# Kernel optimization log

Hardware: AMD Instinct MI355X
Metric: run time of the kernel (lower is better)

## Reference

```python
import jax, jax.numpy as jnp
import numpy as np

B, TH, TS, HS, WS = 16, 1024, 1024, 1024, 1024


def setup_inputs() -> dict:
    key = jax.random.key(0)
    k1, k2, k3, k4 = jax.random.split(key, 4)
    h = jax.random.normal(k1, (B, TH, HS), dtype=jnp.float32)
    s = jax.random.normal(k2, (B, TS, WS), dtype=jnp.float32)
    # nn.Linear params: weight [out, in], bias [out]
    Wh = jax.random.normal(k3, (HS, HS), dtype=jnp.float32) * 0.02
    bh = jnp.zeros((HS,), dtype=jnp.float32)
    Ws = jax.random.normal(k4, (HS, WS), dtype=jnp.float32) * 0.02
    bs = jnp.zeros((HS,), dtype=jnp.float32)
    return {"h": h, "s": s, "Wh": Wh, "bh": bh, "Ws": Ws, "bs": bs}


def reference(h, s, Wh, bh, Ws, bs):
    hp = jnp.einsum('bth,oh->bto', h, Wh) + bh          # [B, TH, HS]
    sp = jnp.einsum('btw,ow->bto', s, Ws) + bs          # [B, TS, HS]
    scores = jnp.einsum('bik,bjk->bij', hp, sp)         # [B, TH, TS]
    b, th, _ = scores.shape
    # faithful to torch: flat-chunk into rows of length TH, softmax over dim 1
    sm = jax.nn.softmax(scores.reshape(-1, th), axis=1).reshape(b, -1, th)  # [B, TS, TH]
    res = jnp.matmul(sm, hp)                            # [B, TS, HS]
    return res.reshape(-1, res.shape[-1])               # [B*TS, HS]
```

## Files before the change

### kernel.cpp

```cpp
#include <hip/hip_runtime.h>
#include <hip/hip_bf16.h>
#include <stdint.h>


typedef _Float16 half_t;
typedef __attribute__((ext_vector_type(8))) _Float16 half8;
typedef __attribute__((ext_vector_type(4))) _Float16 half4;
typedef __attribute__((ext_vector_type(4))) float floatx4;

__device__ __forceinline__ void gl2lds16(const void* g, void* l) {
    __builtin_amdgcn_global_load_lds(
        (const __attribute__((address_space(1))) uint32_t*)(uintptr_t)g,
        (__attribute__((address_space(3))) uint32_t*)(uintptr_t)l,
        16, 0, 0);
}

#define NT16 16

template<int WF32, int WH16, int WH16T>
__global__ __launch_bounds__(512, 2) void gemm256(
    const half_t* __restrict__ A, const half_t* __restrict__ B,
    const float* __restrict__ bias,
    float* __restrict__ Cf, half_t* __restrict__ Ch, half_t* __restrict__ ChT,
    int lda, int ldb, int N,
    long aBatch, long bBatch, long cfBatch, int ldcf)
{
    extern __shared__ char smem[];

    const int tid  = threadIdx.x;
    const int wave = tid >> 6;
    const int lane = tid & 63;
    const int wr = wave >> 2;
    const int wc = wave & 3;
    const int lr = lane & 15, lg = lane >> 4;

    const long batch = blockIdx.z;
    const half_t* Ab = A + batch * aBatch;
    const half_t* Bb = B + batch * bBatch;
    const int row0 = blockIdx.x * 256;
    const int col0 = blockIdx.y * 256;

    floatx4 acc[8][4];
#pragma unroll
    for (int m = 0; m < 8; ++m)
#pragma unroll
        for (int n = 0; n < 4; ++n)
            acc[m][n] = (floatx4){0.f, 0.f, 0.f, 0.f};

    long aOff[2][2], bOff[2][2];
#pragma unroll
    for (int hh = 0; hh < 2; ++hh)
#pragma unroll
        for (int i = 0; i < 2; ++i) {
            const int off = hh * 16384 + i * 8192 + tid * 16;
            const int e = off ^ (((off >> 7) & 7) << 4);
            const int r = e >> 7, cb = e & 127;
            aOff[hh][i] = (long)(row0 + r) * (long)(lda * 2) + cb;
            bOff[hh][i] = (long)(col0 + r) * (long)(ldb * 2) + cb;
        }

    const int wave_s = __builtin_amdgcn_readfirstlane(wave);
    auto stageHalf = [&](int buf, int isA, int hh, int kk) {
#pragma unroll
        for (int i = 0; i < 2; ++i) {
            const char* g = (isA ? (const char*)Ab + aOff[hh][i]
                                 : (const char*)Bb + bOff[hh][i]) + (long)kk * 2;
            gl2lds16(g, smem + buf * 65536 + (isA ? 0 : 32768)
                          + hh * 16384 + i * 8192 + wave_s * 1024);
        }
    };

    uint32_t aof0 = (uint32_t)((wr * 128 + lr) * 128 + ((lg * 16) ^ ((lr & 7) << 4)));
    uint32_t aof1 = (uint32_t)((wr * 128 + lr) * 128 + ((64 + lg * 16) ^ ((lr & 7) << 4)));
    uint32_t bof0 = (uint32_t)(32768 + (wc * 64 + lr) * 128 + ((lg * 16) ^ ((lr & 7) << 4)));
    uint32_t bof1 = (uint32_t)(32768 + (wc * 64 + lr) * 128 + ((64 + lg * 16) ^ ((lr & 7) << 4)));

    stageHalf(0, 1, 0, 0);  stageHalf(0, 1, 1, 0);
    stageHalf(0, 0, 0, 0);  stageHalf(0, 0, 1, 0);
    __syncthreads();

    for (int t = 0; t < NT16; ++t) {
        if (t + 1 < NT16) {
            const int nxt = (t & 1) ^ 1;
            const int k1 = (t + 1) * 64;
            stageHalf(nxt, 1, 0, k1);  stageHalf(nxt, 1, 1, k1);
            stageHalf(nxt, 0, 0, k1);  stageHalf(nxt, 0, 1, k1);
        }

        half8 aF[4][2], bF[4][2];
#pragma unroll
        for (int ni = 0; ni < 4; ++ni) {
            bF[ni][0] = *(const half8*)(smem + bof0 + ni * 2048);
            bF[ni][1] = *(const half8*)(smem + bof1 + ni * 2048);
        }
#pragma unroll
        for (int mi = 0; mi < 4; ++mi) {
            aF[mi][0] = *(const half8*)(smem + aof0 + mi * 2048);
            aF[mi][1] = *(const half8*)(smem + aof1 + mi * 2048);
        }
#pragma unroll
        for (int mi = 0; mi < 4; ++mi)
#pragma unroll
            for (int ni = 0; ni < 4; ++ni)
#pragma unroll
                for (int ks = 0; ks < 2; ++ks)
                    acc[mi][ni] = __builtin_amdgcn_mfma_f32_16x16x32_f16(
                        aF[mi][ks], bF[ni][ks], acc[mi][ni], 0, 0, 0);
#pragma unroll
        for (int mi = 0; mi < 4; ++mi) {
            aF[mi][0] = *(const half8*)(smem + aof0 + (4 + mi) * 2048);
            aF[mi][1] = *(const half8*)(smem + aof1 + (4 + mi) * 2048);
        }
#pragma unroll
        for (int mi = 0; mi < 4; ++mi)
#pragma unroll
            for (int ni = 0; ni < 4; ++ni)
#pragma unroll
                for (int ks = 0; ks < 2; ++ks)
                    acc[4 + mi][ni] = __builtin_amdgcn_mfma_f32_16x16x32_f16(
                        aF[mi][ks], bF[ni][ks], acc[4 + mi][ni], 0, 0, 0);

        __syncthreads();
        aof0 ^= 65536; aof1 ^= 65536; bof0 ^= 65536; bof1 ^= 65536;
    }

    {
        float* wlds = (float*)(smem + wave * 2304);
        float bv[4];
#pragma unroll
        for (int n = 0; n < 4; ++n)
            bv[n] = bias ? bias[col0 + wc * 64 + n * 16 + lr] : 0.f;
        const int er = lane >> 2, ec = lane & 3;
        const int oc = lane >> 1, tc = lane & 1;
#pragma unroll
        for (int m = 0; m < 8; ++m) {
#pragma unroll
            for (int np = 0; np < 2; ++np) {
#pragma unroll
                for (int n2 = 0; n2 < 2; ++n2)
#pragma unroll
                    for (int j = 0; j < 4; ++j)
                        wlds[(lg * 4 + j) * 36 + n2 * 16 + lr] =
                            acc[m][np * 2 + n2][j] + bv[np * 2 + n2];
                const int grow = row0 + wr * 128 + m * 16;
                const int gcol = col0 + wc * 64 + np * 32;
                float4 q0 = *(float4*)&wlds[er * 36 + ec * 8];
                float4 q1 = *(float4*)&wlds[er * 36 + ec * 8 + 4];
                if (WF32) {
                    float* p = Cf + batch * cfBatch + (long)(grow + er) * ldcf + gcol + ec * 8;
                    *(float4*)p = q0;
                    *(float4*)(p + 4) = q1;
                }
                if (WH16) {
                    half8 o = { (half_t)q0.x, (half_t)q0.y, (half_t)q0.z, (half_t)q0.w,
                                (half_t)q1.x, (half_t)q1.y, (half_t)q1.z, (half_t)q1.w };
                    *(half8*)&Ch[(long)(grow + er) * N + gcol + ec * 8] = o;
                }
                if (WH16T) {
                    float tv[8];
#pragma unroll
                    for (int k = 0; k < 8; ++k)
                        tv[k] = wlds[(tc * 8 + k) * 36 + oc];
                    half8 o = { (half_t)tv[0], (half_t)tv[1], (half_t)tv[2], (half_t)tv[3],
                                (half_t)tv[4], (half_t)tv[5], (half_t)tv[6], (half_t)tv[7] };
                    const int gt = grow + tc * 8;
                    *(half8*)&ChT[(long)(gt >> 10) * 1048576
                                  + (long)(gcol + oc) * 1024 + (gt & 1023)] = o;
                }
                __builtin_amdgcn_s_waitcnt(0);
            }
        }
    }
}

__global__ void softmax_inplace(float* __restrict__ S) {
    const long r = blockIdx.x;
    float* row = S + r * 1024;
    const int tid = threadIdx.x;
    const int wave = tid >> 6, lane = tid & 63;

    float4 v = ((const float4*)row)[tid];
    float mx = fmaxf(fmaxf(v.x, v.y), fmaxf(v.z, v.w));
#pragma unroll
    for (int off = 32; off > 0; off >>= 1)
        mx = fmaxf(mx, __shfl_xor(mx, off));
    __shared__ float rmx[4], rsm[4];
    if (lane == 0) rmx[wave] = mx;
    __syncthreads();
    mx = fmaxf(fmaxf(rmx[0], rmx[1]), fmaxf(rmx[2], rmx[3]));

    float e0 = __expf(v.x - mx), e1 = __expf(v.y - mx);
    float e2 = __expf(v.z - mx), e3 = __expf(v.w - mx);
    float s = e0 + e1 + e2 + e3;
#pragma unroll
    for (int off = 32; off > 0; off >>= 1)
        s += __shfl_xor(s, off);
    if (lane == 0) rsm[wave] = s;
    __syncthreads();
    s = rsm[0] + rsm[1] + rsm[2] + rsm[3];

    const float inv = 1.0f / s;
    half4 o = { (half_t)(e0 * inv), (half_t)(e1 * inv), (half_t)(e2 * inv), (half_t)(e3 * inv) };
    ((half4*)((half_t*)S + r * 2048))[tid] = o;
}

__global__ void cvt_f16(const float4* __restrict__ src, half4* __restrict__ dst, int n4) {
    const int stride = gridDim.x * blockDim.x;
    for (int i = blockIdx.x * blockDim.x + threadIdx.x; i < n4; i += stride) {
        float4 v = src[i];
        half4 o = { (half_t)v.x, (half_t)v.y, (half_t)v.z, (half_t)v.w };
        dst[i] = o;
    }
}

extern "C" void kernel_launch(void* const* d_in, const int* in_sizes, int n_in,
                              void* d_out, int out_size, void* d_ws, size_t ws_size,
                              hipStream_t stream) {
    const float* h  = (const float*)d_in[0];
    const float* s  = (const float*)d_in[1];
    const float* Wh = (const float*)d_in[2];
    const float* bh = (const float*)d_in[3];
    const float* Ws = (const float*)d_in[4];
    const float* bs = (const float*)d_in[5];

    const long MB = 16384;
    const long D  = 1024;

    char* w = (char*)d_ws;
    half_t* h16 = (half_t*)w;  w += MB * D * 2;
    half_t* s16 = (half_t*)w;  w += MB * D * 2;
    float*  sc  = (float*)h16;
    half_t* Wh16 = (half_t*)w;  w += D * D * 2;
    half_t* Ws16 = (half_t*)w;  w += D * D * 2;
    half_t* hp16 = (half_t*)w;  w += MB * D * 2;
    half_t* sp16 = (half_t*)w;  w += MB * D * 2;
    half_t* hpT  = (half_t*)w;  w += MB * D * 2;

    hipFuncSetAttribute(reinterpret_cast<const void*>(&gemm256<0,1,1>),
                        hipFuncAttributeMaxDynamicSharedMemorySize, 131072);
    hipFuncSetAttribute(reinterpret_cast<const void*>(&gemm256<0,1,0>),
                        hipFuncAttributeMaxDynamicSharedMemorySize, 131072);
    hipFuncSetAttribute(reinterpret_cast<const void*>(&gemm256<1,0,0>),
                        hipFuncAttributeMaxDynamicSharedMemorySize, 131072);

    cvt_f16<<<512,  256, 0, stream>>>((const float4*)Wh, (half4*)Wh16, (int)(D * D / 4));
    cvt_f16<<<512,  256, 0, stream>>>((const float4*)Ws, (half4*)Ws16, (int)(D * D / 4));
    cvt_f16<<<2048, 256, 0, stream>>>((const float4*)h,  (half4*)h16,  (int)(MB * D / 4));
    cvt_f16<<<2048, 256, 0, stream>>>((const float4*)s,  (half4*)s16,  (int)(MB * D / 4));

    gemm256<0,1,1><<<dim3(64, 4, 1), 512, 131072, stream>>>(
        h16, Wh16, bh, nullptr, hp16, hpT, 1024, 1024, 1024, 0, 0, 0, 0);
    gemm256<0,1,0><<<dim3(64, 4, 1), 512, 131072, stream>>>(
        s16, Ws16, bs, nullptr, sp16, nullptr, 1024, 1024, 1024, 0, 0, 0, 0);
    gemm256<1,0,0><<<dim3(4, 4, 16), 512, 131072, stream>>>(
        hp16, sp16, nullptr, sc, nullptr, nullptr, 1024, 1024, 1024,
        1048576L, 1048576L, 1048576L, 1024);
    softmax_inplace<<<16384, 256, 0, stream>>>(sc);
    gemm256<1,0,0><<<dim3(4, 4, 16), 512, 131072, stream>>>(
        (const half_t*)sc, hpT, nullptr, (float*)d_out, nullptr, nullptr,
        2048, 1024, 1024, 2097152L, 1048576L, 1048576L, 1024);
}
```

Before: 236.8 us.

## Fuse fp32-to-fp16 conversion of activations into projection GEMM A-loads and add XCD block swizzle

```diff
diff --git a/kernel.cpp b/kernel.cpp
--- a/kernel.cpp
+++ b/kernel.cpp
@@ -17,9 +17,10 @@
 
 #define NT16 16
 
-template<int WF32, int WH16, int WH16T>
+template<int WF32, int WH16, int WH16T, int RSA, int SWZ>
 __global__ __launch_bounds__(512, 2) void gemm256(
-    const half_t* __restrict__ A, const half_t* __restrict__ B,
+    const half_t* __restrict__ A, const float* __restrict__ A32,
+    const half_t* __restrict__ B,
     const float* __restrict__ bias,
     float* __restrict__ Cf, half_t* __restrict__ Ch, half_t* __restrict__ ChT,
     int lda, int ldb, int N,
@@ -34,11 +35,21 @@
     const int wc = wave & 3;
     const int lr = lane & 15, lg = lane >> 4;
 
-    const long batch = blockIdx.z;
-    const half_t* Ab = A + batch * aBatch;
+    long batch; int row0, col0;
+    if constexpr (SWZ) {
+        const int lin = blockIdx.x + (blockIdx.y << 2) + (blockIdx.z << 4);
+        const int xcd = lin & 7, per = lin >> 3;
+        batch = (xcd << 1) | (per >> 4);
+        const int wt = per & 15;
+        row0 = (wt & 3) * 256;
+        col0 = (wt >> 2) * 256;
+    } else {
+        batch = blockIdx.z;
+        row0 = blockIdx.x * 256;
+        col0 = blockIdx.y * 256;
+    }
+
     const half_t* Bb = B + batch * bBatch;
-    const int row0 = blockIdx.x * 256;
-    const int col0 = blockIdx.y * 256;
 
     floatx4 acc[8][4];
 #pragma unroll
@@ -47,7 +58,8 @@
         for (int n = 0; n < 4; ++n)
             acc[m][n] = (floatx4){0.f, 0.f, 0.f, 0.f};
 
-    long aOff[2][2], bOff[2][2];
+    long bOff[2][2];
+    long aOffG[2][2];
 #pragma unroll
     for (int hh = 0; hh < 2; ++hh)
 #pragma unroll
@@ -55,36 +67,86 @@
             const int off = hh * 16384 + i * 8192 + tid * 16;
             const int e = off ^ (((off >> 7) & 7) << 4);
             const int r = e >> 7, cb = e & 127;
-            aOff[hh][i] = (long)(row0 + r) * (long)(lda * 2) + cb;
             bOff[hh][i] = (long)(col0 + r) * (long)(ldb * 2) + cb;
+            if constexpr (!RSA)
+                aOffG[hh][i] = (long)(row0 + r) * (long)(lda * 2) + cb;
         }
 
     const int wave_s = __builtin_amdgcn_readfirstlane(wave);
-    auto stageHalf = [&](int buf, int isA, int hh, int kk) {
-#pragma unroll
-        for (int i = 0; i < 2; ++i) {
-            const char* g = (isA ? (const char*)Ab + aOff[hh][i]
-                                 : (const char*)Bb + bOff[hh][i]) + (long)kk * 2;
-            gl2lds16(g, smem + buf * 65536 + (isA ? 0 : 32768)
-                          + hh * 16384 + i * 8192 + wave_s * 1024);
-        }
+    auto stageB = [&](int buf, int kk) {
+#pragma unroll
+        for (int hh = 0; hh < 2; ++hh)
+#pragma unroll
+            for (int i = 0; i < 2; ++i)
+                gl2lds16((const char*)Bb + bOff[hh][i] + (long)kk * 2,
+                         smem + buf * 65536 + 32768 + hh * 16384 + i * 8192 + wave_s * 1024);
     };
+    auto stageA16 = [&](int buf, int kk) {
+        const half_t* Ab = A + batch * aBatch;
+#pragma unroll
+        for (int hh = 0; hh < 2; ++hh)
+#pragma unroll
+            for (int i = 0; i < 2; ++i)
+                gl2lds16((const char*)Ab + aOffG[hh][i] + (long)kk * 2,
+                         smem + buf * 65536 + hh * 16384 + i * 8192 + wave_s * 1024);
+    };
+
+    int rsaRow[4], rsaKb[4];
+#pragma unroll
+    for (int c = 0; c < 4; ++c) {
+        const int off = c * 8192 + tid * 16;
+        rsaRow[c] = off >> 7;
+        rsaKb[c]  = off & 127;
+    }
 
     uint32_t aof0 = (uint32_t)((wr * 128 + lr) * 128 + ((lg * 16) ^ ((lr & 7) << 4)));
     uint32_t aof1 = (uint32_t)((wr * 128 + lr) * 128 + ((64 + lg * 16) ^ ((lr & 7) << 4)));
     uint32_t bof0 = (uint32_t)(32768 + (wc * 64 + lr) * 128 + ((lg * 16) ^ ((lr & 7) << 4)));
     uint32_t bof1 = (uint32_t)(32768 + (wc * 64 + lr) * 128 + ((64 + lg * 16) ^ ((lr & 7) << 4)));
 
-    stageHalf(0, 1, 0, 0);  stageHalf(0, 1, 1, 0);
-    stageHalf(0, 0, 0, 0);  stageHalf(0, 0, 1, 0);
+    auto rsaLoad = [&](float4 (&fv)[4][2], int kk) {
+#pragma unroll
+        for (int c = 0; c < 4; ++c) {
+            const float* src = A32 + batch * aBatch
+                             + (long)(row0 + rsaRow[c]) * lda + kk + (rsaKb[c] >> 1);
+            fv[c][0] = *(const float4*)src;
+            fv[c][1] = *(const float4*)(src + 4);
+        }
+    };
+    auto rsaWrite = [&](float4 (&fv)[4][2], int buf) {
+#pragma unroll
+        for (int c = 0; c < 4; ++c) {
+            half8 o = { (half_t)fv[c][0].x, (half_t)fv[c][0].y, (half_t)fv[c][0].z, (half_t)fv[c][0].w,
+                        (half_t)fv[c][1].x, (half_t)fv[c][1].y, (half_t)fv[c][1].z, (half_t)fv[c][1].w };
+            *(half8*)(smem + buf * 65536 + rsaRow[c] * 128
+                      + (rsaKb[c] ^ ((rsaRow[c] & 7) << 4))) = o;
+        }
+    };
+
+    if constexpr (RSA) {
+        float4 fv[4][2];
+        rsaLoad(fv, 0);
+        stageB(0, 0);
+        rsaWrite(fv, 0);
+    } else {
+        stageA16(0, 0);
+        stageB(0, 0);
+    }
     __syncthreads();
 
     for (int t = 0; t < NT16; ++t) {
+        const int nxt = (t & 1) ^ 1;
+        const int k1 = (t + 1) * 64;
+
+        float4 fv[4][2];
         if (t + 1 < NT16) {
-            const int nxt = (t & 1) ^ 1;
-            const int k1 = (t + 1) * 64;
-            stageHalf(nxt, 1, 0, k1);  stageHalf(nxt, 1, 1, k1);
-            stageHalf(nxt, 0, 0, k1);  stageHalf(nxt, 0, 1, k1);
+            if constexpr (RSA) {
+                rsaLoad(fv, k1);
+                stageB(nxt, k1);
+            } else {
+                stageA16(nxt, k1);
+                stageB(nxt, k1);
+            }
         }
 
         half8 aF[4][2], bF[4][2];
@@ -98,6 +160,9 @@
             aF[mi][0] = *(const half8*)(smem + aof0 + mi * 2048);
             aF[mi][1] = *(const half8*)(smem + aof1 + mi * 2048);
         }
+
+        if (RSA && t + 1 < NT16) rsaWrite(fv, nxt);
+
 #pragma unroll
         for (int mi = 0; mi < 4; ++mi)
 #pragma unroll
@@ -227,36 +292,32 @@
     const long D  = 1024;
 
     char* w = (char*)d_ws;
-    half_t* h16 = (half_t*)w;  w += MB * D * 2;
-    half_t* s16 = (half_t*)w;  w += MB * D * 2;
-    float*  sc  = (float*)h16;
+    float*  sc   = (float*)w;   w += MB * D * 4;
     half_t* Wh16 = (half_t*)w;  w += D * D * 2;
     half_t* Ws16 = (half_t*)w;  w += D * D * 2;
     half_t* hp16 = (half_t*)w;  w += MB * D * 2;
     half_t* sp16 = (half_t*)w;  w += MB * D * 2;
     half_t* hpT  = (half_t*)w;  w += MB * D * 2;
 
-    hipFuncSetAttribute(reinterpret_cast<const void*>(&gemm256<0,1,1>),
+    (void)hipFuncSetAttribute(reinterpret_cast<const void*>(&gemm256<0,1,1,1,0>),
                         hipFuncAttributeMaxDynamicSharedMemorySize, 131072);
-    hipFuncSetAttribute(reinterpret_cast<const void*>(&gemm256<0,1,0>),
+    (void)hipFuncSetAttribute(reinterpret_cast<const void*>(&gemm256<0,1,0,1,0>),
                         hipFuncAttributeMaxDynamicSharedMemorySize, 131072);
-    hipFuncSetAttribute(reinterpret_cast<const void*>(&gemm256<1,0,0>),
+    (void)hipFuncSetAttribute(reinterpret_cast<const void*>(&gemm256<1,0,0,0,1>),
                         hipFuncAttributeMaxDynamicSharedMemorySize, 131072);
 
-    cvt_f16<<<512,  256, 0, stream>>>((const float4*)Wh, (half4*)Wh16, (int)(D * D / 4));
-    cvt_f16<<<512,  256, 0, stream>>>((const float4*)Ws, (half4*)Ws16, (int)(D * D / 4));
-    cvt_f16<<<2048, 256, 0, stream>>>((const float4*)h,  (half4*)h16,  (int)(MB * D / 4));
-    cvt_f16<<<2048, 256, 0, stream>>>((const float4*)s,  (half4*)s16,  (int)(MB * D / 4));
-
-    gemm256<0,1,1><<<dim3(64, 4, 1), 512, 131072, stream>>>(
-        h16, Wh16, bh, nullptr, hp16, hpT, 1024, 1024, 1024, 0, 0, 0, 0);
-    gemm256<0,1,0><<<dim3(64, 4, 1), 512, 131072, stream>>>(
-        s16, Ws16, bs, nullptr, sp16, nullptr, 1024, 1024, 1024, 0, 0, 0, 0);
-    gemm256<1,0,0><<<dim3(4, 4, 16), 512, 131072, stream>>>(
-        hp16, sp16, nullptr, sc, nullptr, nullptr, 1024, 1024, 1024,
+    cvt_f16<<<512, 256, 0, stream>>>((const float4*)Wh, (half4*)Wh16, (int)(D * D / 4));
+    cvt_f16<<<512, 256, 0, stream>>>((const float4*)Ws, (half4*)Ws16, (int)(D * D / 4));
+
+    gemm256<0,1,1,1,0><<<dim3(64, 4, 1), 512, 131072, stream>>>(
+        nullptr, h, Wh16, bh, nullptr, hp16, hpT, 1024, 1024, 1024, 0, 0, 0, 0);
+    gemm256<0,1,0,1,0><<<dim3(64, 4, 1), 512, 131072, stream>>>(
+        nullptr, s, Ws16, bs, nullptr, sp16, nullptr, 1024, 1024, 1024, 0, 0, 0, 0);
+    gemm256<1,0,0,0,1><<<dim3(4, 4, 16), 512, 131072, stream>>>(
+        hp16, nullptr, sp16, nullptr, sc, nullptr, nullptr, 1024, 1024, 1024,
         1048576L, 1048576L, 1048576L, 1024);
     softmax_inplace<<<16384, 256, 0, stream>>>(sc);
-    gemm256<1,0,0><<<dim3(4, 4, 16), 512, 131072, stream>>>(
-        (const half_t*)sc, hpT, nullptr, (float*)d_out, nullptr, nullptr,
+    gemm256<1,0,0,0,1><<<dim3(4, 4, 16), 512, 131072, stream>>>(
+        (const half_t*)sc, nullptr, hpT, nullptr, (float*)d_out, nullptr, nullptr,
         2048, 1024, 1024, 2097152L, 1048576L, 1048576L, 1024);
 }
```

New measurement: 223.2 us. 1.06x faster.

## Use 128x128 tiles for projections and XCD-aware block swizzle for batched GEMMs

Applied to the files above, without the earlier changes.

```diff
diff --git a/kernel.cpp b/kernel.cpp
--- a/kernel.cpp
+++ b/kernel.cpp
@@ -15,113 +15,78 @@
         16, 0, 0);
 }
 
-#define NT16 16
-
-template<int WF32, int WH16, int WH16T>
-__global__ __launch_bounds__(512, 2) void gemm256(
+template<int WH16T>
+__global__ __launch_bounds__(256, 4) void gemm128(
     const half_t* __restrict__ A, const half_t* __restrict__ B,
     const float* __restrict__ bias,
-    float* __restrict__ Cf, half_t* __restrict__ Ch, half_t* __restrict__ ChT,
-    int lda, int ldb, int N,
-    long aBatch, long bBatch, long cfBatch, int ldcf)
+    half_t* __restrict__ Ch, half_t* __restrict__ ChT)
 {
-    extern __shared__ char smem[];
+    __shared__ char smem[32768];
 
     const int tid  = threadIdx.x;
     const int wave = tid >> 6;
     const int lane = tid & 63;
-    const int wr = wave >> 2;
-    const int wc = wave & 3;
+    const int wr = wave >> 1, wc = wave & 1;
     const int lr = lane & 15, lg = lane >> 4;
 
-    const long batch = blockIdx.z;
-    const half_t* Ab = A + batch * aBatch;
-    const half_t* Bb = B + batch * bBatch;
-    const int row0 = blockIdx.x * 256;
-    const int col0 = blockIdx.y * 256;
-
-    floatx4 acc[8][4];
-#pragma unroll
-    for (int m = 0; m < 8; ++m)
+    const int row0 = blockIdx.x * 128;
+    const int col0 = blockIdx.y * 128;
+
+    floatx4 acc[4][4];
+#pragma unroll
+    for (int m = 0; m < 4; ++m)
 #pragma unroll
         for (int n = 0; n < 4; ++n)
             acc[m][n] = (floatx4){0.f, 0.f, 0.f, 0.f};
 
-    long aOff[2][2], bOff[2][2];
-#pragma unroll
-    for (int hh = 0; hh < 2; ++hh)
-#pragma unroll
-        for (int i = 0; i < 2; ++i) {
-            const int off = hh * 16384 + i * 8192 + tid * 16;
-            const int e = off ^ (((off >> 7) & 7) << 4);
-            const int r = e >> 7, cb = e & 127;
-            aOff[hh][i] = (long)(row0 + r) * (long)(lda * 2) + cb;
-            bOff[hh][i] = (long)(col0 + r) * (long)(ldb * 2) + cb;
-        }
-
+    long aOff[2], bOff[2];
+#pragma unroll
+    for (int i = 0; i < 2; ++i) {
+        const int off = i * 4096 + tid * 16;
+        const int e = off ^ (((off >> 7) & 3) << 4);
+        const int r = e >> 6, cb = e & 63;
+        aOff[i] = (long)(row0 + r) * 2048 + cb;
+        bOff[i] = (long)(col0 + r) * 2048 + cb;
+    }
     const int wave_s = __builtin_amdgcn_readfirstlane(wave);
-    auto stageHalf = [&](int buf, int isA, int hh, int kk) {
-#pragma unroll
-        for (int i = 0; i < 2; ++i) {
-            const char* g = (isA ? (const char*)Ab + aOff[hh][i]
-                                 : (const char*)Bb + bOff[hh][i]) + (long)kk * 2;
-            gl2lds16(g, smem + buf * 65536 + (isA ? 0 : 32768)
-                          + hh * 16384 + i * 8192 + wave_s * 1024);
-        }
+
+    auto stage = [&](int buf, int kk) {
+#pragma unroll
+        for (int i = 0; i < 2; ++i)
+            gl2lds16((const char*)A + aOff[i] + (long)kk * 2,
+                     smem + buf * 16384 + i * 4096 + wave_s * 1024);
+#pragma unroll
+        for (int i = 0; i < 2; ++i)
+            gl2lds16((const char*)B + bOff[i] + (long)kk * 2,
+                     smem + buf * 16384 + 8192 + i * 4096 + wave_s * 1024);
     };
 
-    uint32_t aof0 = (uint32_t)((wr * 128 + lr) * 128 + ((lg * 16) ^ ((lr & 7) << 4)));
-    uint32_t aof1 = (uint32_t)((wr * 128 + lr) * 128 + ((64 + lg * 16) ^ ((lr & 7) << 4)));
-    uint32_t bof0 = (uint32_t)(32768 + (wc * 64 + lr) * 128 + ((lg * 16) ^ ((lr & 7) << 4)));
-    uint32_t bof1 = (uint32_t)(32768 + (wc * 64 + lr) * 128 + ((64 + lg * 16) ^ ((lr & 7) << 4)));
-
-    stageHalf(0, 1, 0, 0);  stageHalf(0, 1, 1, 0);
-    stageHalf(0, 0, 0, 0);  stageHalf(0, 0, 1, 0);
+    const uint32_t swx = (uint32_t)((lg * 16) ^ (((lr >> 1) & 3) << 4));
+    uint32_t aof = (uint32_t)((wr * 64 + lr) * 64) + swx;
+    uint32_t bof = 8192u + (uint32_t)((wc * 64 + lr) * 64) + swx;
+
+    stage(0, 0);
     __syncthreads();
 
-    for (int t = 0; t < NT16; ++t) {
-        if (t + 1 < NT16) {
-            const int nxt = (t & 1) ^ 1;
-            const int k1 = (t + 1) * 64;
-            stageHalf(nxt, 1, 0, k1);  stageHalf(nxt, 1, 1, k1);
-            stageHalf(nxt, 0, 0, k1);  stageHalf(nxt, 0, 1, k1);
-        }
-
-        half8 aF[4][2], bF[4][2];
-#pragma unroll
-        for (int ni = 0; ni < 4; ++ni) {
-            bF[ni][0] = *(const half8*)(smem + bof0 + ni * 2048);
-            bF[ni][1] = *(const half8*)(smem + bof1 + ni * 2048);
-        }
-#pragma unroll
-        for (int mi = 0; mi < 4; ++mi) {
-            aF[mi][0] = *(const half8*)(smem + aof0 + mi * 2048);
-            aF[mi][1] = *(const half8*)(smem + aof1 + mi * 2048);
-        }
+    for (int t = 0; t < 32; ++t) {
+        if (t + 1 < 32) stage((t & 1) ^ 1, (t + 1) * 32);
+
+        half8 aF[4], bF[4];
+#pragma unroll
+        for (int ni = 0; ni < 4; ++ni)
+            bF[ni] = *(const half8*)(smem + bof + ni * 1024);
 #pragma unroll
         for (int mi = 0; mi < 4; ++mi)
+            aF[mi] = *(const half8*)(smem + aof + mi * 1024);
+#pragma unroll
+        for (int mi = 0; mi < 4; ++mi)
 #pragma unroll
             for (int ni = 0; ni < 4; ++ni)
-#pragma unroll
-                for (int ks = 0; ks < 2; ++ks)
-                    acc[mi][ni] = __builtin_amdgcn_mfma_f32_16x16x32_f16(
-                        aF[mi][ks], bF[ni][ks], acc[mi][ni], 0, 0, 0);
-#pragma unroll
-        for (int mi = 0; mi < 4; ++mi) {
-            aF[mi][0] = *(const half8*)(smem + aof0 + (4 + mi) * 2048);
-            aF[mi][1] = *(const half8*)(smem + aof1 + (4 + mi) * 2048);
-        }
-#pragma unroll
-        for (int mi = 0; mi < 4; ++mi)
-#pragma unroll
-            for (int ni = 0; ni < 4; ++ni)
-#pragma unroll
-                for (int ks = 0; ks < 2; ++ks)
-                    acc[4 + mi][ni] = __builtin_amdgcn_mfma_f32_16x16x32_f16(
-                        aF[mi][ks], bF[ni][ks], acc[4 + mi][ni], 0, 0, 0);
+                acc[mi][ni] = __builtin_amdgcn_mfma_f32_16x16x32_f16(
+                    aF[mi], bF[ni], acc[mi][ni], 0, 0, 0);
 
         __syncthreads();
-        aof0 ^= 65536; aof1 ^= 65536; bof0 ^= 65536; bof1 ^= 65536;
+        aof ^= 16384; bof ^= 16384;
     }
 
     {
@@ -129,11 +94,11 @@
         float bv[4];
 #pragma unroll
         for (int n = 0; n < 4; ++n)
-            bv[n] = bias ? bias[col0 + wc * 64 + n * 16 + lr] : 0.f;
+            bv[n] = bias[col0 + wc * 64 + n * 16 + lr];
         const int er = lane >> 2, ec = lane & 3;
         const int oc = lane >> 1, tc = lane & 1;
 #pragma unroll
-        for (int m = 0; m < 8; ++m) {
+        for (int m = 0; m < 4; ++m) {
 #pragma unroll
             for (int np = 0; np < 2; ++np) {
 #pragma unroll
@@ -142,19 +107,14 @@
                     for (int j = 0; j < 4; ++j)
                         wlds[(lg * 4 + j) * 36 + n2 * 16 + lr] =
                             acc[m][np * 2 + n2][j] + bv[np * 2 + n2];
-                const int grow = row0 + wr * 128 + m * 16;
+                const int grow = row0 + wr * 64 + m * 16;
                 const int gcol = col0 + wc * 64 + np * 32;
                 float4 q0 = *(float4*)&wlds[er * 36 + ec * 8];
                 float4 q1 = *(float4*)&wlds[er * 36 + ec * 8 + 4];
-                if (WF32) {
-                    float* p = Cf + batch * cfBatch + (long)(grow + er) * ldcf + gcol + ec * 8;
-                    *(float4*)p = q0;
-                    *(float4*)(p + 4) = q1;
-                }
-                if (WH16) {
+                {
                     half8 o = { (half_t)q0.x, (half_t)q0.y, (half_t)q0.z, (half_t)q0.w,
                                 (half_t)q1.x, (half_t)q1.y, (half_t)q1.z, (half_t)q1.w };
-                    *(half8*)&Ch[(long)(grow + er) * N + gcol + ec * 8] = o;
+                    *(half8*)&Ch[(long)(grow + er) * 1024 + gcol + ec * 8] = o;
                 }
                 if (WH16T) {
                     float tv[8];
@@ -173,6 +133,149 @@
     }
 }
 
+#define NT16 16
+
+template<int SWZ>
+__global__ __launch_bounds__(512, 2) void gemm256(
+    const half_t* __restrict__ A, const half_t* __restrict__ B,
+    float* __restrict__ Cf,
+    int lda, int ldb,
+    long aBatch, long bBatch, long cfBatch, int ldcf)
+{
+    extern __shared__ char smem[];
+
+    const int tid  = threadIdx.x;
+    const int wave = tid >> 6;
+    const int lane = tid & 63;
+    const int wr = wave >> 2;
+    const int wc = wave & 3;
+    const int lr = lane & 15, lg = lane >> 4;
+
+    long batch; int row0, col0;
+    if constexpr (SWZ) {
+        const int lin = blockIdx.x + (blockIdx.y << 2) + (blockIdx.z << 4);
+        const int xcd = lin & 7, per = lin >> 3;
+        batch = (xcd << 1) | (per >> 4);
+        const int wt = per & 15;
+        row0 = (wt & 3) * 256;
+        col0 = (wt >> 2) * 256;
+    } else {
+        batch = blockIdx.z;
+        row0 = blockIdx.x * 256;
+        col0 = blockIdx.y * 256;
+    }
+
+    const half_t* Ab = A + batch * aBatch;
+    const half_t* Bb = B + batch * bBatch;
+
+    floatx4 acc[8][4];
+#pragma unroll
+    for (int m = 0; m < 8; ++m)
+#pragma unroll
+        for (int n = 0; n < 4; ++n)
+            acc[m][n] = (floatx4){0.f, 0.f, 0.f, 0.f};
+
+    long aOff[2][2], bOff[2][2];
+#pragma unroll
+    for (int hh = 0; hh < 2; ++hh)
+#pragma unroll
+        for (int i = 0; i < 2; ++i) {
+            const int off = hh * 16384 + i * 8192 + tid * 16;
+            const int e = off ^ (((off >> 7) & 7) << 4);
+            const int r = e >> 7, cb = e & 127;
+            aOff[hh][i] = (long)(row0 + r) * (long)(lda * 2) + cb;
+            bOff[hh][i] = (long)(col0 + r) * (long)(ldb * 2) + cb;
+        }
+
+    const int wave_s = __builtin_amdgcn_readfirstlane(wave);
+    auto stage = [&](int buf, int kk) {
+#pragma unroll
+        for (int hh = 0; hh < 2; ++hh)
+#pragma unroll
+            for (int i = 0; i < 2; ++i)
+                gl2lds16((const char*)Ab + aOff[hh][i] + (long)kk * 2,
+                         smem + buf * 65536 + hh * 16384 + i * 8192 + wave_s * 1024);
+#pragma unroll
+        for (int hh = 0; hh < 2; ++hh)
+#pragma unroll
+            for (int i = 0; i < 2; ++i)
+                gl2lds16((const char*)Bb + bOff[hh][i] + (long)kk * 2,
+                         smem + buf * 65536 + 32768 + hh * 16384 + i * 8192 + wave_s * 1024);
+    };
+
+    uint32_t aof0 = (uint32_t)((wr * 128 + lr) * 128 + ((lg * 16) ^ ((lr & 7) << 4)));
+    uint32_t aof1 = (uint32_t)((wr * 128 + lr) * 128 + ((64 + lg * 16) ^ ((lr & 7) << 4)));
+    uint32_t bof0 = (uint32_t)(32768 + (wc * 64 + lr) * 128 + ((lg * 16) ^ ((lr & 7) << 4)));
+    uint32_t bof1 = (uint32_t)(32768 + (wc * 64 + lr) * 128 + ((64 + lg * 16) ^ ((lr & 7) << 4)));
+
+    stage(0, 0);
+    __syncthreads();
+
+    for (int t = 0; t < NT16; ++t) {
+        if (t + 1 < NT16) stage((t & 1) ^ 1, (t + 1) * 64);
+
+        half8 aF[4][2], bF[4][2];
+#pragma unroll
+        for (int ni = 0; ni < 4; ++ni) {
+            bF[ni][0] = *(const half8*)(smem + bof0 + ni * 2048);
+            bF[ni][1] = *(const half8*)(smem + bof1 + ni * 2048);
+        }
+#pragma unroll
+        for (int mi = 0; mi < 4; ++mi) {
+            aF[mi][0] = *(const half8*)(smem + aof0 + mi * 2048);
+            aF[mi][1] = *(const half8*)(smem + aof1 + mi * 2048);
+        }
+#pragma unroll
+        for (int mi = 0; mi < 4; ++mi)
+#pragma unroll
+            for (int ni = 0; ni < 4; ++ni)
+#pragma unroll
+                for (int ks = 0; ks < 2; ++ks)
+                    acc[mi][ni] = __builtin_amdgcn_mfma_f32_16x16x32_f16(
+                        aF[mi][ks], bF[ni][ks], acc[mi][ni], 0, 0, 0);
+#pragma unroll
+        for (int mi = 0; mi < 4; ++mi) {
+            aF[mi][0] = *(const half8*)(smem + aof0 + (4 + mi) * 2048);
+            aF[mi][1] = *(const half8*)(smem + aof1 + (4 + mi) * 2048);
+        }
+#pragma unroll
+        for (int mi = 0; mi < 4; ++mi)
+#pragma unroll
+            for (int ni = 0; ni < 4; ++ni)
+#pragma unroll
+                for (int ks = 0; ks < 2; ++ks)
+                    acc[4 + mi][ni] = __builtin_amdgcn_mfma_f32_16x16x32_f16(
+                        aF[mi][ks], bF[ni][ks], acc[4 + mi][ni], 0, 0, 0);
+
+        __syncthreads();
+        aof0 ^= 65536; aof1 ^= 65536; bof0 ^= 65536; bof1 ^= 65536;
+    }
+
+    {
+        float* wlds = (float*)(smem + wave * 2304);
+        const int er = lane >> 2, ec = lane & 3;
+#pragma unroll
+        for (int m = 0; m < 8; ++m) {
+#pragma unroll
+            for (int np = 0; np < 2; ++np) {
+#pragma unroll
+                for (int n2 = 0; n2 < 2; ++n2)
+#pragma unroll
+                    for (int j = 0; j < 4; ++j)
+                        wlds[(lg * 4 + j) * 36 + n2 * 16 + lr] = acc[m][np * 2 + n2][j];
+                const int grow = row0 + wr * 128 + m * 16;
+                const int gcol = col0 + wc * 64 + np * 32;
+                float4 q0 = *(float4*)&wlds[er * 36 + ec * 8];
+                float4 q1 = *(float4*)&wlds[er * 36 + ec * 8 + 4];
+                float* p = Cf + batch * cfBatch + (long)(grow + er) * ldcf + gcol + ec * 8;
+                *(float4*)p = q0;
+                *(float4*)(p + 4) = q1;
+                __builtin_amdgcn_s_waitcnt(0);
+            }
+        }
+    }
+}
+
 __global__ void softmax_inplace(float* __restrict__ S) {
     const long r = blockIdx.x;
     float* row = S + r * 1024;
@@ -227,20 +330,16 @@
     const long D  = 1024;
 
     char* w = (char*)d_ws;
-    half_t* h16 = (half_t*)w;  w += MB * D * 2;
-    half_t* s16 = (half_t*)w;  w += MB * D * 2;
-    float*  sc  = (float*)h16;
+    float*  sc   = (float*)w;   w += MB * D * 4;
     half_t* Wh16 = (half_t*)w;  w += D * D * 2;
     half_t* Ws16 = (half_t*)w;  w += D * D * 2;
+    half_t* h16  = (half_t*)w;  w += MB * D * 2;
+    half_t* s16  = (half_t*)w;  w += MB * D * 2;
     half_t* hp16 = (half_t*)w;  w += MB * D * 2;
     half_t* sp16 = (half_t*)w;  w += MB * D * 2;
     half_t* hpT  = (half_t*)w;  w += MB * D * 2;
 
-    hipFuncSetAttribute(reinterpret_cast<const void*>(&gemm256<0,1,1>),
-                        hipFuncAttributeMaxDynamicSharedMemorySize, 131072);
-    hipFuncSetAttribute(reinterpret_cast<const void*>(&gemm256<0,1,0>),
-                        hipFuncAttributeMaxDynamicSharedMemorySize, 131072);
-    hipFuncSetAttribute(reinterpret_cast<const void*>(&gemm256<1,0,0>),
+    (void)hipFuncSetAttribute(reinterpret_cast<const void*>(&gemm256<1>),
                         hipFuncAttributeMaxDynamicSharedMemorySize, 131072);
 
     cvt_f16<<<512,  256, 0, stream>>>((const float4*)Wh, (half4*)Wh16, (int)(D * D / 4));
@@ -248,15 +347,12 @@
     cvt_f16<<<2048, 256, 0, stream>>>((const float4*)h,  (half4*)h16,  (int)(MB * D / 4));
     cvt_f16<<<2048, 256, 0, stream>>>((const float4*)s,  (half4*)s16,  (int)(MB * D / 4));
 
-    gemm256<0,1,1><<<dim3(64, 4, 1), 512, 131072, stream>>>(
-        h16, Wh16, bh, nullptr, hp16, hpT, 1024, 1024, 1024, 0, 0, 0, 0);
-    gemm256<0,1,0><<<dim3(64, 4, 1), 512, 131072, stream>>>(
-        s16, Ws16, bs, nullptr, sp16, nullptr, 1024, 1024, 1024, 0, 0, 0, 0);
-    gemm256<1,0,0><<<dim3(4, 4, 16), 512, 131072, stream>>>(
-        hp16, sp16, nullptr, sc, nullptr, nullptr, 1024, 1024, 1024,
-        1048576L, 1048576L, 1048576L, 1024);
+    gemm128<1><<<dim3(128, 8), 256, 0, stream>>>(h16, Wh16, bh, hp16, hpT);
+    gemm128<0><<<dim3(128, 8), 256, 0, stream>>>(s16, Ws16, bs, sp16, nullptr);
+    gemm256<1><<<dim3(4, 4, 16), 512, 131072, stream>>>(
+        hp16, sp16, sc, 1024, 1024, 1048576L, 1048576L, 1048576L, 1024);
     softmax_inplace<<<16384, 256, 0, stream>>>(sc);
-    gemm256<1,0,0><<<dim3(4, 4, 16), 512, 131072, stream>>>(
-        (const half_t*)sc, hpT, nullptr, (float*)d_out, nullptr, nullptr,
-        2048, 1024, 1024, 2097152L, 1048576L, 1048576L, 1024);
-}
+    gemm256<1><<<dim3(4, 4, 16), 512, 131072, stream>>>(
+        (const half_t*)sc, hpT, (float*)d_out, 2048, 1024,
+        2097152L, 1048576L, 1048576L, 1024);
+}
```

Measured after the change: 247.8 us. 4.7% more time.
